# Kernel tuning notes

Measured on AMD Instinct MI355X. Metric: run time of the kernel, lower is better.

## Reference

```python
import jax, jax.numpy as jnp
import numpy as np

VOCAB, EMBED, HIDDEN, LAYERS = 128, 256, 512, 2
B, T = 64, 512


def setup_inputs() -> dict:
    key = jax.random.key(0)
    ks = jax.random.split(key, 10)
    x = jax.random.randint(ks[0], (B, T), 0, VOCAB)
    emb = jax.random.normal(ks[1], (VOCAB, EMBED), jnp.float32) * 0.02
    emb = emb.at[0].set(0.0)  # padding_idx=0
    inp = {"x": x, "embedding": emb}
    in_dims = [EMBED, HIDDEN]
    for l in range(LAYERS):
        s = 1.0 / np.sqrt(in_dims[l])
        inp[f"W_xh{l}"] = jax.random.uniform(ks[2 + 3 * l], (HIDDEN, in_dims[l]), jnp.float32, -s, s)
        # orthogonal-ish init for W_hh
        a = jax.random.normal(ks[3 + 3 * l], (HIDDEN, HIDDEN), jnp.float32)
        q, _ = jnp.linalg.qr(a)
        inp[f"W_hh{l}"] = q
        inp[f"b_h{l}"] = jnp.zeros((HIDDEN,), jnp.float32)
    s = 1.0 / np.sqrt(HIDDEN)
    inp["W_hy"] = jax.random.uniform(ks[8], (VOCAB, HIDDEN), jnp.float32, -s, s)
    inp["b_y"] = jax.random.uniform(ks[9], (VOCAB,), jnp.float32, -s, s)
    return inp


def _rnn_layer(layer_in, W_xh, W_hh, b_h):
    # layer_in: (B, T, D). Precompute input projection for all t, scan recurrence.
    xW = jnp.einsum('btd,hd->bth', layer_in, W_xh) + b_h  # (B, T, H)
    h0 = jnp.zeros((layer_in.shape[0], W_hh.shape[0]), layer_in.dtype)

    def step(h_prev, xW_t):
        h_t = jnp.tanh(xW_t + h_prev @ W_hh.T)
        return h_t, h_t

    h_last, hs = jax.lax.scan(step, h0, jnp.swapaxes(xW, 0, 1))  # hs: (T, B, H)
    return jnp.swapaxes(hs, 0, 1), h_last


def reference(x, embedding, W_xh0, W_hh0, b_h0, W_xh1, W_hh1, b_h1, W_hy, b_y):
    layer_in = embedding[x]  # (B, T, E)
    hidden = []
    for W_xh, W_hh, b_h in ((W_xh0, W_hh0, b_h0), (W_xh1, W_hh1, b_h1)):
        layer_in, h_last = _rnn_layer(layer_in, W_xh, W_hh, b_h)
        hidden.append(h_last)
    logits = jnp.einsum('bth,vh->btv', layer_in, W_hy) + b_y
    return (logits, *hidden)
```

## Files before the change

kernel.cpp:

```cpp
#include <hip/hip_runtime.h>
#include <hip/hip_fp16.h>

typedef _Float16 f16x8 __attribute__((ext_vector_type(8)));
typedef float f32x4 __attribute__((ext_vector_type(4)));
typedef unsigned int u32x4 __attribute__((ext_vector_type(4)));
typedef unsigned int u32x2 __attribute__((ext_vector_type(2)));
typedef unsigned long long u64;

static constexpr int T_SEQ = 512;
static constexpr int BATCH = 64;
static constexpr int HID   = 512;
static constexpr int VOC   = 128;

static constexpr int AOFF_EMB  = 0;
static constexpr int AOFF_WXH0 = 32768;
static constexpr int AOFF_WHH0 = 163840;
static constexpr int AOFF_WXH1 = 425984;
static constexpr int AOFF_WHH1 = 688128;
static constexpr int AOFF_WHY  = 950272;
static constexpr int ATOT      = 1015808;

static constexpr size_t OFF_RING   = 16384;
static constexpr size_t RING_BYTES = 32ull * 4 * 512 * 16;
static constexpr size_t OFF_HIST   = OFF_RING + RING_BYTES;
static constexpr size_t HIST_BYTES = 512ull * 16 * 512 * 16;
static constexpr size_t OFF_ARENA  = OFF_HIST + HIST_BYTES;
static constexpr size_t OFF_XW0    = OFF_ARENA + 2ull * ATOT;
static constexpr size_t PLANE_B    = (size_t)T_SEQ * BATCH * HID * 2;
static constexpr size_t OFF_H1A    = OFF_XW0 + PLANE_B;

__device__ __forceinline__ unsigned short h2u(_Float16 h) {
  union { _Float16 h; unsigned short u; } c; c.h = h; return c.u;
}
__device__ __forceinline__ _Float16 u2h(unsigned short u) {
  union { unsigned short u; _Float16 h; } c; c.u = u; return c.h;
}
__device__ __forceinline__ float fast_tanh(float x) {
  float e = __expf(2.0f * x);
  return 1.0f - 2.0f * __builtin_amdgcn_rcpf(e + 1.0f);
}

__device__ __forceinline__ void store16_sys(u64* addr, u64 data, unsigned tag) {
  u32x4 v;
  v.x = (unsigned)data; v.y = (unsigned)(data >> 32);
  v.z = tag;            v.w = 0u;
  asm volatile("global_store_dwordx4 %0, %1, off sc0 sc1"
               :: "v"(addr), "v"(v) : "memory");
}
__device__ __forceinline__ void issue3x16(const u64* a, const u64* b, const u64* c,
                                          u32x4& v0, u32x4& v1, u32x4& v2) {
  asm volatile("global_load_dwordx4 %0, %3, off sc0 sc1\n\t"
               "global_load_dwordx4 %1, %4, off sc0 sc1\n\t"
               "global_load_dwordx4 %2, %5, off sc0 sc1"
               : "=&v"(v0), "=&v"(v1), "=&v"(v2)
               : "v"(a), "v"(b), "v"(c)
               : "memory");
}
__device__ __forceinline__ void issue4x16(const u64* a, const u64* b, const u64* c,
                                          const u64* d, u32x4& v0, u32x4& v1,
                                          u32x4& v2, u32x4& v3) {
  asm volatile("global_load_dwordx4 %0, %4, off sc0 sc1\n\t"
               "global_load_dwordx4 %1, %5, off sc0 sc1\n\t"
               "global_load_dwordx4 %2, %6, off sc0 sc1\n\t"
               "global_load_dwordx4 %3, %7, off sc0 sc1"
               : "=&v"(v0), "=&v"(v1), "=&v"(v2), "=&v"(v3)
               : "v"(a), "v"(b), "v"(c), "v"(d)
               : "memory");
}
__device__ __forceinline__ void wait3(u32x4& v0, u32x4& v1, u32x4& v2) {
  asm volatile("s_waitcnt vmcnt(0)" : "+v"(v0), "+v"(v1), "+v"(v2) :: "memory");
}
__device__ __forceinline__ void wait4_v3(u32x4& v0, u32x4& v1, u32x4& v2, u32x4& v3) {
  asm volatile("s_waitcnt vmcnt(3)" : "+v"(v0), "+v"(v1), "+v"(v2), "+v"(v3) :: "memory");
}
__device__ __forceinline__ void wait4_v0(u32x4& v0, u32x4& v1, u32x4& v2, u32x4& v3) {
  asm volatile("s_waitcnt vmcnt(0)" : "+v"(v0), "+v"(v1), "+v"(v2), "+v"(v3) :: "memory");
}
__device__ __forceinline__ void load3x16_sys(const u64* a, const u64* b, const u64* c,
                                             u32x4& v0, u32x4& v1, u32x4& v2) {
  asm volatile("global_load_dwordx4 %0, %3, off sc0 sc1\n\t"
               "global_load_dwordx4 %1, %4, off sc0 sc1\n\t"
               "global_load_dwordx4 %2, %5, off sc0 sc1\n\t"
               "s_waitcnt vmcnt(0)"
               : "=&v"(v0), "=&v"(v1), "=&v"(v2)
               : "v"(a), "v"(b), "v"(c)
               : "memory");
}
__device__ __forceinline__ void load4x16_sys(const u64* a, const u64* b, const u64* c,
                                             const u64* d, u32x4& v0, u32x4& v1,
                                             u32x4& v2, u32x4& v3) {
  asm volatile("global_load_dwordx4 %0, %4, off sc0 sc1\n\t"
               "global_load_dwordx4 %1, %5, off sc0 sc1\n\t"
               "global_load_dwordx4 %2, %6, off sc0 sc1\n\t"
               "global_load_dwordx4 %3, %7, off sc0 sc1\n\t"
               "s_waitcnt vmcnt(0)"
               : "=&v"(v0), "=&v"(v1), "=&v"(v2), "=&v"(v3)
               : "v"(a), "v"(b), "v"(c), "v"(d)
               : "memory");
}

__global__ __launch_bounds__(256) void canon_kernel(
    const float* p0, const float* p1, const float* p2, const float* p3,
    const float* p4, const float* p5, _Float16* __restrict__ dst,
    int* __restrict__ ringhist) {
  const int NZ = (int)((RING_BYTES + HIST_BYTES) / 4);
  for (int i = blockIdx.x * 256 + threadIdx.x; i < NZ; i += gridDim.x * 256)
    ringhist[i] = 0;
  const float* srcs[6] = {p0, p1, p2, p3, p4, p5};
  const int ns[6] = {32768, 131072, 262144, 262144, 262144, 65536};
  for (int i = blockIdx.x * 256 + threadIdx.x; i < ATOT; i += gridDim.x * 256) {
    int off = i, s = 0;
    while (off >= ns[s]) { off -= ns[s]; ++s; }
    dst[i] = (_Float16)srcs[s][off];
  }
}

__global__ __launch_bounds__(256) void xw0_kernel(
    const int* __restrict__ x, const _Float16* __restrict__ emb,
    const _Float16* __restrict__ Wxh, const float* __restrict__ bh,
    _Float16* __restrict__ xwf) {
  __shared__ _Float16 Bs[64][264];
  const int t = blockIdx.x, n0 = blockIdx.y * 64, tid = threadIdx.x;
#pragma unroll
  for (int rep = 0; rep < 8; ++rep) {
    int flat = rep * 256 + tid;
    int row = flat >> 5, c8 = flat & 31;
    *(f16x8*)&Bs[row][c8 * 8] = *(const f16x8*)&Wxh[(size_t)(n0 + row) * 256 + c8 * 8];
  }
  __syncthreads();
  const int wv = tid >> 6, lane = tid & 63, l15 = lane & 15, quad = lane >> 4;
  const int b = wv * 16 + l15;
  const int idx = x[b * 512 + t];
  f32x4 acc[4];
#pragma unroll
  for (int nt = 0; nt < 4; ++nt) { float bv = bh[n0 + nt * 16 + l15]; acc[nt] = {bv, bv, bv, bv}; }
#pragma unroll
  for (int kc = 0; kc < 8; ++kc) {
    f16x8 a = *(const f16x8*)&emb[(size_t)idx * 256 + kc * 32 + quad * 8];
#pragma unroll
    for (int nt = 0; nt < 4; ++nt) {
      f16x8 bf = *(const f16x8*)&Bs[nt * 16 + l15][kc * 32 + quad * 8];
      acc[nt] = __builtin_amdgcn_mfma_f32_16x16x32_f16(a, bf, acc[nt], 0, 0, 0);
    }
  }
#pragma unroll
  for (int nt = 0; nt < 4; ++nt) {
    unsigned int lo = (unsigned int)h2u((_Float16)acc[nt][0]) |
                      ((unsigned int)h2u((_Float16)acc[nt][1]) << 16);
    unsigned int hi = (unsigned int)h2u((_Float16)acc[nt][2]) |
                      ((unsigned int)h2u((_Float16)acc[nt][3]) << 16);
    u32x2 pk = {lo, hi};
    *(u32x2*)&xwf[(size_t)t * 32768 + (size_t)(n0 + nt * 16 + l15) * 64 + wv * 16 + quad * 4] = pk;
  }
}

__device__ __forceinline__ void layer0_loop(
    const _Float16* __restrict__ Whh, const _Float16* __restrict__ xwf,
    u64* __restrict__ ring, u64* __restrict__ hist,
    _Float16* alds, const int g, const int q, const int tid) {
  u64* aldsu = (u64*)alds;
  const int lane = tid & 63, wv = tid >> 6, l15 = lane & 15, quad = lane >> 4;
  const int n0 = q * 128 + wv * 16;

  u32x4 Bw[16];
#pragma unroll
  for (int i = 0; i < 16; ++i) {
    const int kc = (q * 4 + i) & 15;
    Bw[i] = *(const u32x4*)&Whh[(size_t)(n0 + l15) * 512 + kc * 32 + quad * 8];
  }
#pragma unroll
  for (int i = 0; i < 16; ++i)
    asm volatile("" : "+v"(Bw[i]));

  u64* pring[3];
  int pquar[3];
  {
    int pi = 0;
    for (int qq = 0; qq < 4; ++qq)
      if (qq != q) { pring[pi] = ring + (size_t)(g * 4 + qq) * 4096; pquar[pi] = qq; ++pi; }
  }
  u64* myring = ring + (size_t)(g * 4 + q) * 4096;

  const _Float16* xwb = xwf + (size_t)(n0 + l15) * 64 + g * 16 + quad * 4;
  u32x2 pfx = *(const u32x2*)xwb;

  for (int t = 0; t < T_SEQ; ++t) {
    f32x4 acc;
    acc[0] = (float)u2h((unsigned short)(pfx.x & 0xFFFFu));
    acc[1] = (float)u2h((unsigned short)(pfx.x >> 16));
    acc[2] = (float)u2h((unsigned short)(pfx.y & 0xFFFFu));
    acc[3] = (float)u2h((unsigned short)(pfx.y >> 16));
    if (t + 1 < T_SEQ) pfx = *(const u32x2*)(xwb + (size_t)(t + 1) * 32768);

    if (t > 0) {
      const int slot = (t - 1) & 3;
      const u64* a0 = pring[0] + (size_t)slot * 1024 + tid * 2;
      const u64* a1 = pring[1] + (size_t)slot * 1024 + tid * 2;
      const u64* a2 = pring[2] + (size_t)slot * 1024 + tid * 2;
      u32x4 r0, r1, r2;
      issue3x16(a0, a1, a2, r0, r1, r2);

#pragma unroll
      for (int i = 0; i < 4; ++i) {
        const int kc = q * 4 + i;
        f16x8 a = *(const f16x8*)&alds[kc * 512 + lane * 8];
        acc = __builtin_amdgcn_mfma_f32_16x16x32_f16(
            a, __builtin_bit_cast(f16x8, Bw[i]), acc, 0, 0, 0);
      }

      wait3(r0, r1, r2);
      const unsigned wtag = (unsigned)t;
      while ((r0.z != wtag) | (r1.z != wtag) | (r2.z != wtag))
        load3x16_sys(a0, a1, a2, r0, r1, r2);

      aldsu[pquar[0] * 512 + tid] = ((u64)r0.y << 32) | r0.x;
      aldsu[pquar[1] * 512 + tid] = ((u64)r1.y << 32) | r1.x;
      aldsu[pquar[2] * 512 + tid] = ((u64)r2.y << 32) | r2.x;
      __syncthreads();

#pragma unroll
      for (int i = 4; i < 16; ++i) {
        const int kc = (q * 4 + i) & 15;
        f16x8 a = *(const f16x8*)&alds[kc * 512 + lane * 8];
        acc = __builtin_amdgcn_mfma_f32_16x16x32_f16(
            a, __builtin_bit_cast(f16x8, Bw[i]), acc, 0, 0, 0);
      }
      __syncthreads();
    }

    {
      const int n = n0 + l15;
      const int kc = n >> 5, qd = (n >> 3) & 3, j = n & 7;
#pragma unroll
      for (int r = 0; r < 4; ++r)
        alds[kc * 512 + (qd * 16 + quad * 4 + r) * 8 + j] = (_Float16)fast_tanh(acc[r]);
    }
    __syncthreads();
    {
      u64 v = aldsu[q * 512 + tid];
      store16_sys(myring + (size_t)(t & 3) * 1024 + tid * 2, v, (unsigned)(t + 1));
      store16_sys(hist + ((size_t)(t * 16 + g * 4 + q) * 512 + tid) * 2, v,
                  (unsigned)(t + 1));
    }
  }
}

__device__ __forceinline__ void layer1_loop(
    const _Float16* __restrict__ Whh, const _Float16* __restrict__ Wxh,
    const float* __restrict__ bh, const u64* __restrict__ hist,
    u64* __restrict__ ring, _Float16* __restrict__ h1A,
    _Float16* alds, _Float16* xlds, const int g, const int q, const int tid) {
  u64* aldsu = (u64*)alds;
  u64* xldsu = (u64*)xlds;
  const int lane = tid & 63, wv = tid >> 6, l15 = lane & 15, quad = lane >> 4;
  const int n0 = q * 128 + wv * 16;

  u32x4 Bh[16], Bx[16];
#pragma unroll
  for (int i = 0; i < 16; ++i) {
    const int kc = (q * 4 + i) & 15;
    Bh[i] = *(const u32x4*)&Whh[(size_t)(n0 + l15) * 512 + kc * 32 + quad * 8];
  }
#pragma unroll
  for (int i = 0; i < 16; ++i)
    Bx[i] = *(const u32x4*)&Wxh[(size_t)(n0 + l15) * 512 + i * 32 + quad * 8];
#pragma unroll
  for (int i = 0; i < 16; ++i) {
    asm volatile("" : "+v"(Bh[i]));
    asm volatile("" : "+v"(Bx[i]));
  }
  const float bv = bh[n0 + l15];

  u64* pring[3];
  int pquar[3];
  {
    int pi = 0;
    for (int qq = 0; qq < 4; ++qq)
      if (qq != q) { pring[pi] = ring + (size_t)(16 + g * 4 + qq) * 4096; pquar[pi] = qq; ++pi; }
  }
  u64* myring = ring + (size_t)(16 + g * 4 + q) * 4096;

  for (int u = 0; u < T_SEQ; ++u) {
    f32x4 acc = {bv, bv, bv, bv};
    const unsigned htag = (unsigned)(u + 1);

    const u64* hb = hist + ((size_t)(u * 16 + g * 4) * 512 + tid) * 2;
    const u64* h0a = hb, *h1a = hb + 1024, *h2a = hb + 2048, *h3a = hb + 3072;
    const int slot = (u - 1) & 3;
    const u64* a0 = pring[0] + (size_t)slot * 1024 + tid * 2;
    const u64* a1 = pring[1] + (size_t)slot * 1024 + tid * 2;
    const u64* a2 = pring[2] + (size_t)slot * 1024 + tid * 2;
    u32x4 hv0, hv1, hv2, hv3, r0, r1, r2;

    issue4x16(h0a, h1a, h2a, h3a, hv0, hv1, hv2, hv3);
    if (u > 0) {
      issue3x16(a0, a1, a2, r0, r1, r2);
#pragma unroll
      for (int i = 0; i < 4; ++i) {
        const int kc = q * 4 + i;
        f16x8 a = *(const f16x8*)&alds[kc * 512 + lane * 8];
        acc = __builtin_amdgcn_mfma_f32_16x16x32_f16(
            a, __builtin_bit_cast(f16x8, Bh[i]), acc, 0, 0, 0);
      }
      wait4_v3(hv0, hv1, hv2, hv3);
    } else {
      wait4_v0(hv0, hv1, hv2, hv3);
    }
    if (__any((hv0.z != htag) | (hv1.z != htag) | (hv2.z != htag) | (hv3.z != htag))) {
      do {
        load4x16_sys(h0a, h1a, h2a, h3a, hv0, hv1, hv2, hv3);
      } while (__any((hv0.z != htag) | (hv1.z != htag) |
                     (hv2.z != htag) | (hv3.z != htag)));
      if (u > 0) issue3x16(a0, a1, a2, r0, r1, r2);
    }
    xldsu[0 * 512 + tid] = ((u64)hv0.y << 32) | hv0.x;
    xldsu[1 * 512 + tid] = ((u64)hv1.y << 32) | hv1.x;
    xldsu[2 * 512 + tid] = ((u64)hv2.y << 32) | hv2.x;
    xldsu[3 * 512 + tid] = ((u64)hv3.y << 32) | hv3.x;
    __syncthreads();

#pragma unroll
    for (int kc = 0; kc < 16; ++kc) {
      f16x8 a = *(const f16x8*)&xlds[kc * 512 + lane * 8];
      acc = __builtin_amdgcn_mfma_f32_16x16x32_f16(
          a, __builtin_bit_cast(f16x8, Bx[kc]), acc, 0, 0, 0);
    }

    if (u > 0) {
      const unsigned wtag = (unsigned)u;
      wait3(r0, r1, r2);
      while ((r0.z != wtag) | (r1.z != wtag) | (r2.z != wtag))
        load3x16_sys(a0, a1, a2, r0, r1, r2);
      aldsu[pquar[0] * 512 + tid] = ((u64)r0.y << 32) | r0.x;
      aldsu[pquar[1] * 512 + tid] = ((u64)r1.y << 32) | r1.x;
      aldsu[pquar[2] * 512 + tid] = ((u64)r2.y << 32) | r2.x;
      __syncthreads();

      if (q == 0) {
        u64* dst = (u64*)h1A + ((size_t)(u - 1) * 4 + g) * 2048;
#pragma unroll
        for (int i = 0; i < 4; ++i)
          dst[tid + 512 * i] = aldsu[tid + 512 * i];
      }
#pragma unroll
      for (int i = 4; i < 16; ++i) {
        const int kc = (q * 4 + i) & 15;
        f16x8 a = *(const f16x8*)&alds[kc * 512 + lane * 8];
        acc = __builtin_amdgcn_mfma_f32_16x16x32_f16(
            a, __builtin_bit_cast(f16x8, Bh[i]), acc, 0, 0, 0);
      }
    }
    __syncthreads();
    {
      const int n = n0 + l15;
      const int kc = n >> 5, qd = (n >> 3) & 3, j = n & 7;
#pragma unroll
      for (int r = 0; r < 4; ++r)
        alds[kc * 512 + (qd * 16 + quad * 4 + r) * 8 + j] = (_Float16)fast_tanh(acc[r]);
    }
    __syncthreads();
    {
      u64 v = aldsu[q * 512 + tid];
      store16_sys(myring + (size_t)(u & 3) * 1024 + tid * 2, v, (unsigned)(u + 1));
    }
  }

  if (q == 0) {
    const int slot = (T_SEQ - 1) & 3;
    const u64* a0 = pring[0] + (size_t)slot * 1024 + tid * 2;
    const u64* a1 = pring[1] + (size_t)slot * 1024 + tid * 2;
    const u64* a2 = pring[2] + (size_t)slot * 1024 + tid * 2;
    u32x4 r0, r1, r2;
    load3x16_sys(a0, a1, a2, r0, r1, r2);
    const unsigned wtag = (unsigned)T_SEQ;
    while ((r0.z != wtag) | (r1.z != wtag) | (r2.z != wtag))
      load3x16_sys(a0, a1, a2, r0, r1, r2);
    aldsu[pquar[0] * 512 + tid] = ((u64)r0.y << 32) | r0.x;
    aldsu[pquar[1] * 512 + tid] = ((u64)r1.y << 32) | r1.x;
    aldsu[pquar[2] * 512 + tid] = ((u64)r2.y << 32) | r2.x;
    __syncthreads();
    u64* dst = (u64*)h1A + ((size_t)(T_SEQ - 1) * 4 + g) * 2048;
#pragma unroll
    for (int i = 0; i < 4; ++i)
      dst[tid + 512 * i] = aldsu[tid + 512 * i];
  }
}

__global__ __launch_bounds__(512, 2) void rnn_fused_kernel(
    const _Float16* __restrict__ Whh0, const _Float16* __restrict__ xwf0,
    const _Float16* __restrict__ Whh1, const _Float16* __restrict__ Wxh1,
    const float* __restrict__ bh1,
    u64* __restrict__ ring, u64* __restrict__ hist, _Float16* __restrict__ h1A) {
  __shared__ _Float16 lds[32 * 512];
  const int bid = blockIdx.x, tid = threadIdx.x;
  if (bid < 16) {
    layer0_loop(Whh0, xwf0, ring, hist, lds, bid & 3, bid >> 2, tid);
  } else {
    const int b = bid - 16;
    layer1_loop(Whh1, Wxh1, bh1, hist, ring, h1A, lds, lds + 16 * 512,
                b & 3, b >> 2, tid);
  }
}

__global__ __launch_bounds__(256) void logits_kernel(
    const _Float16* __restrict__ h1A, const _Float16* __restrict__ Why,
    const float* __restrict__ by, float* __restrict__ out) {
  const int t = blockIdx.x;
  const int wv = threadIdx.x >> 6, lane = threadIdx.x & 63;
  const int l15 = lane & 15, quad = lane >> 4, bb = wv * 16;
  f32x4 acc[8];
#pragma unroll
  for (int vt = 0; vt < 8; ++vt) { float bvv = by[vt * 16 + l15]; acc[vt] = {bvv, bvv, bvv, bvv}; }
#pragma unroll
  for (int kc = 0; kc < 16; ++kc) {
    f16x8 a = *(const f16x8*)&h1A[(((size_t)t * 4 + wv) * 16 + kc) * 512 + lane * 8];
#pragma unroll
    for (int vt = 0; vt < 8; ++vt) {
      f16x8 b = *(const f16x8*)&Why[(size_t)(vt * 16 + l15) * 512 + kc * 32 + quad * 8];
      acc[vt] = __builtin_amdgcn_mfma_f32_16x16x32_f16(a, b, acc[vt], 0, 0, 0);
    }
  }
#pragma unroll
  for (int vt = 0; vt < 8; ++vt)
#pragma unroll
    for (int r = 0; r < 4; ++r)
      out[((size_t)(bb + quad * 4 + r) * 512 + t) * 128 + vt * 16 + l15] = acc[vt][r];
}

__global__ void hlast_kernel(const u64* __restrict__ hist,
                             const _Float16* __restrict__ h1A,
                             float* __restrict__ out) {
  const size_t LOG = (size_t)BATCH * T_SEQ * VOC;
  const size_t HL = (size_t)BATCH * HID;
  int tid = blockIdx.x * 256 + threadIdx.x;
  if (tid < (int)HL) {
    const int b = tid >> 9, n = tid & 511;
    const int gg = b >> 4, m = b & 15;
    const int kc = n >> 5, qd = (n >> 3) & 3, j = n & 7;
    const int pf = kc * 512 + (qd * 16 + m) * 8 + j;
    const int p = pf >> 2;
    const u64 d = hist[(((size_t)(T_SEQ - 1) * 16 + gg * 4 + (p >> 9)) * 512 + (p & 511)) * 2];
    out[LOG + tid] = (float)u2h((unsigned short)(d >> ((pf & 3) * 16)));
    const size_t idx = (((size_t)(T_SEQ - 1) * 4 + gg) * 16 + kc) * 512 + (qd * 16 + m) * 8 + j;
    out[LOG + HL + tid] = (float)h1A[idx];
  }
}

extern "C" void kernel_launch(void* const* d_in, const int* in_sizes, int n_in,
                              void* d_out, int out_size, void* d_ws, size_t ws_size,
                              hipStream_t stream) {
  const int* x = (const int*)d_in[0];
  float* out = (float*)d_out;
  char* ws = (char*)d_ws;
  u64* ring = (u64*)(ws + OFF_RING);
  u64* hist = (u64*)(ws + OFF_HIST);
  _Float16* arena = (_Float16*)(ws + OFF_ARENA);
  _Float16* xw0f = (_Float16*)(ws + OFF_XW0);
  _Float16* h1A  = (_Float16*)(ws + OFF_H1A);

  canon_kernel<<<512, 256, 0, stream>>>(
      (const float*)d_in[1], (const float*)d_in[2], (const float*)d_in[3],
      (const float*)d_in[5], (const float*)d_in[6], (const float*)d_in[8],
      arena, (int*)ring);

  xw0_kernel<<<dim3(512, 8), 256, 0, stream>>>(
      x, arena + AOFF_EMB, arena + AOFF_WXH0, (const float*)d_in[4], xw0f);

  rnn_fused_kernel<<<32, 512, 0, stream>>>(
      arena + AOFF_WHH0, xw0f,
      arena + AOFF_WHH1, arena + AOFF_WXH1, (const float*)d_in[7],
      ring, hist, h1A);

  logits_kernel<<<512, 256, 0, stream>>>(
      h1A, arena + AOFF_WHY, (const float*)d_in[9], out);

  hlast_kernel<<<(BATCH * HID + 255) / 256, 256, 0, stream>>>(hist, h1A, out);
}
```

Measured before the change: 1.279 ms.

## Drop layer-0 ring, split MFMA accumulators, publish hidden state before barrier

Layer 0 now reads peer hidden-state slices directly from the history buffer instead of a separate ring, which removes one system-scope store per step. The MFMA chains are split across several independent accumulators to shorten the dependent-instruction chain on the recurrent critical path. The cross-block publish store is moved ahead of the trailing __syncthreads (guarded by an lgkmcnt wait), and layer 1 writes h1A straight from registers so the LDS copy-out is gone. Launch bounds now allow one block per CU and the register-pinning asm moves inside the loop, which may change register allocation and the order of the floating-point sums.

```diff
diff --git a/kernel.cpp b/kernel.cpp
--- a/kernel.cpp
+++ b/kernel.cpp
@@ -156,8 +156,7 @@
 
 __device__ __forceinline__ void layer0_loop(
     const _Float16* __restrict__ Whh, const _Float16* __restrict__ xwf,
-    u64* __restrict__ ring, u64* __restrict__ hist,
-    _Float16* alds, const int g, const int q, const int tid) {
+    u64* __restrict__ hist, _Float16* alds, const int g, const int q, const int tid) {
   u64* aldsu = (u64*)alds;
   const int lane = tid & 63, wv = tid >> 6, l15 = lane & 15, quad = lane >> 4;
   const int n0 = q * 128 + wv * 16;
@@ -168,35 +167,32 @@
     const int kc = (q * 4 + i) & 15;
     Bw[i] = *(const u32x4*)&Whh[(size_t)(n0 + l15) * 512 + kc * 32 + quad * 8];
   }
-#pragma unroll
-  for (int i = 0; i < 16; ++i)
-    asm volatile("" : "+v"(Bw[i]));
-
-  u64* pring[3];
+
   int pquar[3];
   {
     int pi = 0;
     for (int qq = 0; qq < 4; ++qq)
-      if (qq != q) { pring[pi] = ring + (size_t)(g * 4 + qq) * 4096; pquar[pi] = qq; ++pi; }
-  }
-  u64* myring = ring + (size_t)(g * 4 + q) * 4096;
+      if (qq != q) pquar[pi++] = qq;
+  }
 
   const _Float16* xwb = xwf + (size_t)(n0 + l15) * 64 + g * 16 + quad * 4;
   u32x2 pfx = *(const u32x2*)xwb;
 
   for (int t = 0; t < T_SEQ; ++t) {
-    f32x4 acc;
-    acc[0] = (float)u2h((unsigned short)(pfx.x & 0xFFFFu));
-    acc[1] = (float)u2h((unsigned short)(pfx.x >> 16));
-    acc[2] = (float)u2h((unsigned short)(pfx.y & 0xFFFFu));
-    acc[3] = (float)u2h((unsigned short)(pfx.y >> 16));
+#pragma unroll
+    for (int i = 0; i < 16; ++i) asm volatile("" : "+v"(Bw[i]));
+
+    f32x4 accA, accB = {0.f, 0.f, 0.f, 0.f};
+    accA[0] = (float)u2h((unsigned short)(pfx.x & 0xFFFFu));
+    accA[1] = (float)u2h((unsigned short)(pfx.x >> 16));
+    accA[2] = (float)u2h((unsigned short)(pfx.y & 0xFFFFu));
+    accA[3] = (float)u2h((unsigned short)(pfx.y >> 16));
     if (t + 1 < T_SEQ) pfx = *(const u32x2*)(xwb + (size_t)(t + 1) * 32768);
 
     if (t > 0) {
-      const int slot = (t - 1) & 3;
-      const u64* a0 = pring[0] + (size_t)slot * 1024 + tid * 2;
-      const u64* a1 = pring[1] + (size_t)slot * 1024 + tid * 2;
-      const u64* a2 = pring[2] + (size_t)slot * 1024 + tid * 2;
+      const u64* a0 = hist + (((size_t)(t - 1) * 16 + g * 4 + pquar[0]) * 512 + tid) * 2;
+      const u64* a1 = hist + (((size_t)(t - 1) * 16 + g * 4 + pquar[1]) * 512 + tid) * 2;
+      const u64* a2 = hist + (((size_t)(t - 1) * 16 + g * 4 + pquar[2]) * 512 + tid) * 2;
       u32x4 r0, r1, r2;
       issue3x16(a0, a1, a2, r0, r1, r2);
 
@@ -204,8 +200,8 @@
       for (int i = 0; i < 4; ++i) {
         const int kc = q * 4 + i;
         f16x8 a = *(const f16x8*)&alds[kc * 512 + lane * 8];
-        acc = __builtin_amdgcn_mfma_f32_16x16x32_f16(
-            a, __builtin_bit_cast(f16x8, Bw[i]), acc, 0, 0, 0);
+        accA = __builtin_amdgcn_mfma_f32_16x16x32_f16(
+            a, __builtin_bit_cast(f16x8, Bw[i]), accA, 0, 0, 0);
       }
 
       wait3(r0, r1, r2);
@@ -222,26 +218,32 @@
       for (int i = 4; i < 16; ++i) {
         const int kc = (q * 4 + i) & 15;
         f16x8 a = *(const f16x8*)&alds[kc * 512 + lane * 8];
-        acc = __builtin_amdgcn_mfma_f32_16x16x32_f16(
-            a, __builtin_bit_cast(f16x8, Bw[i]), acc, 0, 0, 0);
+        if (i & 1)
+          accB = __builtin_amdgcn_mfma_f32_16x16x32_f16(
+              a, __builtin_bit_cast(f16x8, Bw[i]), accB, 0, 0, 0);
+        else
+          accA = __builtin_amdgcn_mfma_f32_16x16x32_f16(
+              a, __builtin_bit_cast(f16x8, Bw[i]), accA, 0, 0, 0);
       }
       __syncthreads();
     }
 
     {
+      f32x4 s = accA + accB;
       const int n = n0 + l15;
       const int kc = n >> 5, qd = (n >> 3) & 3, j = n & 7;
 #pragma unroll
       for (int r = 0; r < 4; ++r)
-        alds[kc * 512 + (qd * 16 + quad * 4 + r) * 8 + j] = (_Float16)fast_tanh(acc[r]);
+        alds[kc * 512 + (qd * 16 + quad * 4 + r) * 8 + j] = (_Float16)fast_tanh(s[r]);
+    }
+    asm volatile("s_waitcnt lgkmcnt(0)" ::: "memory");
+    __builtin_amdgcn_sched_barrier(0);
+    {
+      u64 msg = aldsu[q * 512 + tid];
+      store16_sys(hist + (((size_t)t * 16 + g * 4 + q) * 512 + tid) * 2,
+                  msg, (unsigned)(t + 1));
     }
     __syncthreads();
-    {
-      u64 v = aldsu[q * 512 + tid];
-      store16_sys(myring + (size_t)(t & 3) * 1024 + tid * 2, v, (unsigned)(t + 1));
-      store16_sys(hist + ((size_t)(t * 16 + g * 4 + q) * 512 + tid) * 2, v,
-                  (unsigned)(t + 1));
-    }
   }
 }
 
@@ -264,11 +266,6 @@
 #pragma unroll
   for (int i = 0; i < 16; ++i)
     Bx[i] = *(const u32x4*)&Wxh[(size_t)(n0 + l15) * 512 + i * 32 + quad * 8];
-#pragma unroll
-  for (int i = 0; i < 16; ++i) {
-    asm volatile("" : "+v"(Bh[i]));
-    asm volatile("" : "+v"(Bx[i]));
-  }
   const float bv = bh[n0 + l15];
 
   u64* pring[3];
@@ -281,7 +278,14 @@
   u64* myring = ring + (size_t)(16 + g * 4 + q) * 4096;
 
   for (int u = 0; u < T_SEQ; ++u) {
-    f32x4 acc = {bv, bv, bv, bv};
+#pragma unroll
+    for (int i = 0; i < 16; ++i) asm volatile("" : "+v"(Bh[i]));
+#pragma unroll
+    for (int i = 0; i < 16; ++i) asm volatile("" : "+v"(Bx[i]));
+
+    f32x4 accA = {bv, bv, bv, bv};
+    f32x4 accB = {0.f, 0.f, 0.f, 0.f}, accC = {0.f, 0.f, 0.f, 0.f},
+          accD = {0.f, 0.f, 0.f, 0.f};
     const unsigned htag = (unsigned)(u + 1);
 
     const u64* hb = hist + ((size_t)(u * 16 + g * 4) * 512 + tid) * 2;
@@ -299,8 +303,8 @@
       for (int i = 0; i < 4; ++i) {
         const int kc = q * 4 + i;
         f16x8 a = *(const f16x8*)&alds[kc * 512 + lane * 8];
-        acc = __builtin_amdgcn_mfma_f32_16x16x32_f16(
-            a, __builtin_bit_cast(f16x8, Bh[i]), acc, 0, 0, 0);
+        accA = __builtin_amdgcn_mfma_f32_16x16x32_f16(
+            a, __builtin_bit_cast(f16x8, Bh[i]), accA, 0, 0, 0);
       }
       wait4_v3(hv0, hv1, hv2, hv3);
     } else {
@@ -322,8 +326,12 @@
 #pragma unroll
     for (int kc = 0; kc < 16; ++kc) {
       f16x8 a = *(const f16x8*)&xlds[kc * 512 + lane * 8];
-      acc = __builtin_amdgcn_mfma_f32_16x16x32_f16(
-          a, __builtin_bit_cast(f16x8, Bx[kc]), acc, 0, 0, 0);
+      if (kc < 8)
+        accB = __builtin_amdgcn_mfma_f32_16x16x32_f16(
+            a, __builtin_bit_cast(f16x8, Bx[kc]), accB, 0, 0, 0);
+      else
+        accC = __builtin_amdgcn_mfma_f32_16x16x32_f16(
+            a, __builtin_bit_cast(f16x8, Bx[kc]), accC, 0, 0, 0);
     }
 
     if (u > 0) {
@@ -331,38 +339,48 @@
       wait3(r0, r1, r2);
       while ((r0.z != wtag) | (r1.z != wtag) | (r2.z != wtag))
         load3x16_sys(a0, a1, a2, r0, r1, r2);
+
+      if (q == 0) {
+        u64* dplane = (u64*)h1A + ((size_t)(u - 1) * 4 + g) * 2048;
+        dplane[pquar[0] * 512 + tid] = ((u64)r0.y << 32) | r0.x;
+        dplane[pquar[1] * 512 + tid] = ((u64)r1.y << 32) | r1.x;
+        dplane[pquar[2] * 512 + tid] = ((u64)r2.y << 32) | r2.x;
+      }
       aldsu[pquar[0] * 512 + tid] = ((u64)r0.y << 32) | r0.x;
       aldsu[pquar[1] * 512 + tid] = ((u64)r1.y << 32) | r1.x;
       aldsu[pquar[2] * 512 + tid] = ((u64)r2.y << 32) | r2.x;
       __syncthreads();
 
-      if (q == 0) {
-        u64* dst = (u64*)h1A + ((size_t)(u - 1) * 4 + g) * 2048;
-#pragma unroll
-        for (int i = 0; i < 4; ++i)
-          dst[tid + 512 * i] = aldsu[tid + 512 * i];
-      }
 #pragma unroll
       for (int i = 4; i < 16; ++i) {
         const int kc = (q * 4 + i) & 15;
         f16x8 a = *(const f16x8*)&alds[kc * 512 + lane * 8];
-        acc = __builtin_amdgcn_mfma_f32_16x16x32_f16(
-            a, __builtin_bit_cast(f16x8, Bh[i]), acc, 0, 0, 0);
+        if (i & 1)
+          accD = __builtin_amdgcn_mfma_f32_16x16x32_f16(
+              a, __builtin_bit_cast(f16x8, Bh[i]), accD, 0, 0, 0);
+        else
+          accA = __builtin_amdgcn_mfma_f32_16x16x32_f16(
+              a, __builtin_bit_cast(f16x8, Bh[i]), accA, 0, 0, 0);
       }
     }
     __syncthreads();
     {
+      f32x4 s = (accA + accD) + (accB + accC);
       const int n = n0 + l15;
       const int kc = n >> 5, qd = (n >> 3) & 3, j = n & 7;
 #pragma unroll
       for (int r = 0; r < 4; ++r)
-        alds[kc * 512 + (qd * 16 + quad * 4 + r) * 8 + j] = (_Float16)fast_tanh(acc[r]);
+        alds[kc * 512 + (qd * 16 + quad * 4 + r) * 8 + j] = (_Float16)fast_tanh(s[r]);
+    }
+    asm volatile("s_waitcnt lgkmcnt(0)" ::: "memory");
+    __builtin_amdgcn_sched_barrier(0);
+    {
+      u64 msg = aldsu[q * 512 + tid];
+      store16_sys(myring + (size_t)(u & 3) * 1024 + tid * 2, msg, (unsigned)(u + 1));
+      if (q == 0)
+        ((u64*)h1A)[((size_t)u * 4 + g) * 2048 + tid] = msg;
     }
     __syncthreads();
-    {
-      u64 v = aldsu[q * 512 + tid];
-      store16_sys(myring + (size_t)(u & 3) * 1024 + tid * 2, v, (unsigned)(u + 1));
-    }
   }
 
   if (q == 0) {
@@ -375,18 +393,14 @@
     const unsigned wtag = (unsigned)T_SEQ;
     while ((r0.z != wtag) | (r1.z != wtag) | (r2.z != wtag))
       load3x16_sys(a0, a1, a2, r0, r1, r2);
-    aldsu[pquar[0] * 512 + tid] = ((u64)r0.y << 32) | r0.x;
-    aldsu[pquar[1] * 512 + tid] = ((u64)r1.y << 32) | r1.x;
-    aldsu[pquar[2] * 512 + tid] = ((u64)r2.y << 32) | r2.x;
-    __syncthreads();
-    u64* dst = (u64*)h1A + ((size_t)(T_SEQ - 1) * 4 + g) * 2048;
-#pragma unroll
-    for (int i = 0; i < 4; ++i)
-      dst[tid + 512 * i] = aldsu[tid + 512 * i];
-  }
-}
-
-__global__ __launch_bounds__(512, 2) void rnn_fused_kernel(
+    u64* dplane = (u64*)h1A + ((size_t)(T_SEQ - 1) * 4 + g) * 2048;
+    dplane[pquar[0] * 512 + tid] = ((u64)r0.y << 32) | r0.x;
+    dplane[pquar[1] * 512 + tid] = ((u64)r1.y << 32) | r1.x;
+    dplane[pquar[2] * 512 + tid] = ((u64)r2.y << 32) | r2.x;
+  }
+}
+
+__global__ __launch_bounds__(512, 1) void rnn_fused_kernel(
     const _Float16* __restrict__ Whh0, const _Float16* __restrict__ xwf0,
     const _Float16* __restrict__ Whh1, const _Float16* __restrict__ Wxh1,
     const float* __restrict__ bh1,
@@ -394,7 +408,7 @@
   __shared__ _Float16 lds[32 * 512];
   const int bid = blockIdx.x, tid = threadIdx.x;
   if (bid < 16) {
-    layer0_loop(Whh0, xwf0, ring, hist, lds, bid & 3, bid >> 2, tid);
+    layer0_loop(Whh0, xwf0, hist, lds, bid & 3, bid >> 2, tid);
   } else {
     const int b = bid - 16;
     layer1_loop(Whh1, Wxh1, bh1, hist, ring, h1A, lds, lds + 16 * 512,
```

New measurement: 1.198 ms. 1.07x faster.
